# Kernel tuning notes

Hardware: AMD Instinct MI355X
Metric: run time of the kernel (lower is better)

Reference implementation:

```python
import jax, jax.numpy as jnp
import numpy as np

DIM = 512
HEADS = 16
WS = (2, 7, 7)
N = WS[0] * WS[1] * WS[2]  # 98
NW = 64  # number of windows in mask
B_ = 512  # num_windows * batch
HEAD_DIM = DIM // HEADS
SCALE = HEAD_DIM ** -0.5
TABLE = (2 * WS[0] - 1) * (2 * WS[1] - 1) * (2 * WS[2] - 1)  # 507


def _relative_position_index():
    # Faithful to the repo (note: middle coord is NOT multiplied by (2*Ww-1),
    # matching the source exactly).
    ct, ch, cw = np.arange(WS[0]), np.arange(WS[1]), np.arange(WS[2])
    coords = np.stack(np.meshgrid(ct, ch, cw, indexing='ij'))  # [3,Th,Tw,Tw]
    flat = coords.reshape(3, -1)  # [3,N]
    rel = flat[:, :, None] - flat[:, None, :]  # [3,N,N]
    rel = rel.transpose(1, 2, 0).copy()  # [N,N,3]
    rel[:, :, 0] += WS[0] - 1
    rel[:, :, 1] += WS[1] - 1
    rel[:, :, 2] += WS[2] - 1
    rel[:, :, 0] *= (2 * WS[1] - 1) * (2 * WS[2] - 1)
    return rel.sum(-1).astype(np.int32)  # [N,N]


def setup_inputs() -> dict:
    key = jax.random.key(0)
    ks = jax.random.split(key, 7)
    x = jax.random.normal(ks[0], (B_, N, DIM), dtype=jnp.float32)
    mask = jnp.zeros((NW, N, N), dtype=jnp.float32)
    qkv_w = jax.random.normal(ks[1], (3 * DIM, DIM), dtype=jnp.float32) * (DIM ** -0.5)
    qkv_b = jnp.zeros((3 * DIM,), dtype=jnp.float32)
    proj_w = jax.random.normal(ks[2], (DIM, DIM), dtype=jnp.float32) * (DIM ** -0.5)
    proj_b = jnp.zeros((DIM,), dtype=jnp.float32)
    bias_table = jax.random.normal(ks[3], (TABLE, HEADS), dtype=jnp.float32) * 0.02
    rel_index = jnp.asarray(_relative_position_index())
    return {"x": x, "mask": mask, "qkv_w": qkv_w, "qkv_b": qkv_b,
            "proj_w": proj_w, "proj_b": proj_b, "bias_table": bias_table,
            "rel_index": rel_index}


def reference(x, mask, qkv_w, qkv_b, proj_w, proj_b, bias_table, rel_index):
    Bw, n, c = x.shape
    # QKV projection -> [3, B_, H, N, hd]
    qkv = (x @ qkv_w.T + qkv_b).reshape(Bw, n, 3, HEADS, HEAD_DIM)
    qkv = qkv.transpose(2, 0, 3, 1, 4)
    q, k, v = qkv[0], qkv[1], qkv[2]
    attn = jnp.einsum('bhnd,bhmd->bhnm', q * SCALE, k)  # [B_,H,N,N]
    # Gathered relative position bias -> [H,N,N]
    bias = bias_table[rel_index.reshape(-1)].reshape(n, n, HEADS).transpose(2, 0, 1)
    attn = attn + bias[None]
    # Broadcast mask over batch groups of nW windows
    nW = mask.shape[0]
    attn = attn.reshape(Bw // nW, nW, HEADS, n, n) + mask[None, :, None]
    attn = attn.reshape(Bw, HEADS, n, n)
    attn = jax.nn.softmax(attn, axis=-1)
    out = jnp.einsum('bhnm,bhmd->bhnd', attn, v)
    out = out.transpose(0, 2, 1, 3).reshape(Bw, n, c)
    return out @ proj_w.T + proj_b
```

## Files before the change

### kernel.cpp

```cpp
#include <hip/hip_runtime.h>
#include <stdint.h>

#define HEADS 16
#define NTOK 98
#define HD 32
#define SCALE_Q 0.17677669529663687f

typedef __attribute__((ext_vector_type(4))) float floatx4;
typedef __attribute__((ext_vector_type(8))) short shortx8;

__device__ __forceinline__ unsigned short f2bf(float f) {
  union { float f; unsigned u; } v; v.f = f;
  unsigned r = v.u + 0x7fffu + ((v.u >> 16) & 1u);
  return (unsigned short)(r >> 16);
}
__device__ __forceinline__ float bf2f(unsigned short s) {
  union { unsigned u; float f; } v; v.u = ((unsigned)s) << 16;
  return v.f;
}

__device__ __forceinline__ void gload_lds16(const void* g, void* l) {
  __builtin_amdgcn_global_load_lds(
      (const __attribute__((address_space(1))) unsigned int*)g,
      (__attribute__((address_space(3))) unsigned int*)l, 16, 0, 0);
}

__global__ void convert_x_kernel(const float* __restrict__ x,
                                 unsigned short* __restrict__ xbf) {
  int idx = blockIdx.x * 256 + threadIdx.x;
  const float4 f0 = *(const float4*)(x + (size_t)idx * 8);
  const float4 f1 = *(const float4*)(x + (size_t)idx * 8 + 4);
  union { ushort us[8]; uint4 u4; } pk;
  pk.us[0] = f2bf(f0.x); pk.us[1] = f2bf(f0.y);
  pk.us[2] = f2bf(f0.z); pk.us[3] = f2bf(f0.w);
  pk.us[4] = f2bf(f1.x); pk.us[5] = f2bf(f1.y);
  pk.us[6] = f2bf(f1.z); pk.us[7] = f2bf(f1.w);
  *(uint4*)(xbf + (size_t)idx * 8) = pk.u4;
}

__global__ void convert_w_kernel(const float* __restrict__ qkv_w,
                                 const float* __restrict__ proj_w,
                                 unsigned short* __restrict__ wq,
                                 unsigned short* __restrict__ wp) {
  int idx = blockIdx.x * 256 + threadIdx.x;
  if (idx < 1536 * 512) wq[idx] = f2bf(qkv_w[idx]);
  if (idx < 512 * 512) wp[idx] = f2bf(proj_w[idx]);
}

__global__ void bmprep_kernel(const float* __restrict__ table,
                              const int* __restrict__ rel,
                              const float* __restrict__ mask,
                              unsigned short* __restrict__ biasF,
                              unsigned short* __restrict__ maskF) {
  int idx = blockIdx.x * 256 + threadIdx.x;
  if (idx < 229376) {
    int e = idx & 31, lane = (idx >> 5) & 63;
    int rest = idx >> 11;
    int mt = rest % 7, h = rest / 7;
    int nt = e >> 2, r = e & 3;
    int i = mt * 16 + ((lane >> 4) << 2) + r;
    int j = (nt << 4) + (lane & 15);
    int ii = i < NTOK ? i : 97, jj = j < NTOK ? j : 97;
    float v = (nt < 7) ? table[rel[ii * NTOK + jj] * HEADS + h] : 0.f;
    biasF[idx] = f2bf(v);
  } else {
    int t = idx - 229376;
    int e = t & 31, lane = (t >> 5) & 63;
    int rest = t >> 11;
    int mt = rest % 7, wdx = rest / 7;
    int nt = e >> 2, r = e & 3;
    int i = mt * 16 + ((lane >> 4) << 2) + r;
    int j = (nt << 4) + (lane & 15);
    float v;
    if (nt >= 7) v = 0.f;
    else if (j >= NTOK) v = -1e30f;
    else {
      int ii = i < NTOK ? i : 97;
      v = mask[wdx * (NTOK * NTOK) + ii * NTOK + j];
    }
    maskF[t] = f2bf(v);
  }
}

__global__ __launch_bounds__(512, 2)
void qkv_gemm_kernel(const unsigned short* __restrict__ xbf,
                     const unsigned short* __restrict__ wbf,
                     const float* __restrict__ qkv_b,
                     unsigned short* __restrict__ q_out,
                     unsigned short* __restrict__ k_out,
                     unsigned short* __restrict__ v_out) {
  __shared__ unsigned short As[3][128 * 32];
  __shared__ unsigned short Bs[3][256 * 32];
  const int tid = threadIdx.x;
  const int wave = tid >> 6, lane = tid & 63;
  const int id = blockIdx.x;
  const int xc = id & 7, tt = id >> 3;
  const int m0 = (xc * 49 + tt / 6) * 128, n0 = (tt % 6) * 256;
  const int wm = wave & 1, wn = wave >> 1;
  const int ln15 = lane & 15, qd = lane >> 4;
  const int bl_r = lane >> 2, bl_s = lane & 3;

  const int sg_st = bl_s ^ ((bl_r >> 1) & 3);
  const int swz_rd = (qd ^ ((ln15 >> 1) & 3)) * 8;

  const unsigned short* aG = xbf + (size_t)(m0 + wave * 16 + bl_r) * 512 + sg_st * 8;
  const unsigned short* bG0 = wbf + (size_t)(n0 + wave * 32 + bl_r) * 512 + sg_st * 8;
  const unsigned short* bG1 = wbf + (size_t)(n0 + wave * 32 + 16 + bl_r) * 512 + sg_st * 8;

#define QSTAGE(bufi, kk)                                                        \
  do {                                                                          \
    gload_lds16((const void*)(aG + (kk)), (void*)&As[bufi][wave * 512]);        \
    gload_lds16((const void*)(bG0 + (kk)), (void*)&Bs[bufi][wave * 1024]);      \
    gload_lds16((const void*)(bG1 + (kk)), (void*)&Bs[bufi][wave * 1024 + 512]);\
  } while (0)

  QSTAGE(0, 0);
  QSTAGE(1, 32);

  floatx4 acc[4][4] = {};
#pragma unroll
  for (int it = 0; it < 16; ++it) {
    if (it == 15) asm volatile("s_waitcnt vmcnt(0)" ::: "memory");
    else          asm volatile("s_waitcnt vmcnt(3)" ::: "memory");
    __builtin_amdgcn_sched_barrier(0);
    __builtin_amdgcn_s_barrier();
    __builtin_amdgcn_sched_barrier(0);
    if (it + 2 < 16) QSTAGE((it + 2) % 3, (it + 2) * 32);
    const unsigned short* Ab = As[it % 3];
    const unsigned short* Bb = Bs[it % 3];
    shortx8 afrag[4], bfrag[4];
#pragma unroll
    for (int mt = 0; mt < 4; ++mt)
      afrag[mt] = *(const shortx8*)&Ab[(wm * 64 + mt * 16 + ln15) * 32 + swz_rd];
#pragma unroll
    for (int nt = 0; nt < 4; ++nt)
      bfrag[nt] = *(const shortx8*)&Bb[(wn * 64 + nt * 16 + ln15) * 32 + swz_rd];
    __builtin_amdgcn_s_setprio(1);
#pragma unroll
    for (int mt = 0; mt < 4; ++mt)
#pragma unroll
      for (int nt = 0; nt < 4; ++nt)
        acc[mt][nt] = __builtin_amdgcn_mfma_f32_16x16x32_bf16(
            afrag[mt], bfrag[nt], acc[mt][nt], 0, 0, 0);
    __builtin_amdgcn_s_setprio(0);
  }
#undef QSTAGE

  const int which = n0 >> 9;
  unsigned short* __restrict__ outp =
      (which == 0) ? q_out : ((which == 1) ? k_out : v_out);
  const float sc = (which == 0) ? SCALE_Q : 1.0f;
#pragma unroll
  for (int mt = 0; mt < 4; ++mt) {
#pragma unroll
    for (int r = 0; r < 4; ++r) {
      int grow = m0 + wm * 64 + mt * 16 + qd * 4 + r;
      unsigned b = (unsigned)grow / 98u;
      unsigned i = (unsigned)grow - b * 98u;
#pragma unroll
      for (int nt = 0; nt < 4; ++nt) {
        int col = n0 + wn * 64 + nt * 16 + ln15;
        float val = (acc[mt][nt][r] + qkv_b[col]) * sc;
        int h = (col >> 5) & 15;
        int d = col & 31;
        size_t oidx = ((size_t)(b * 16 + h) * 98 + i) * 32 + d;
        outp[oidx] = f2bf(val);
      }
    }
  }
}

__global__ __launch_bounds__(448, 6)
void attn_kernel(const unsigned short* __restrict__ qg,
                 const unsigned short* __restrict__ kg,
                 const unsigned short* __restrict__ vg,
                 const unsigned short* __restrict__ biasF,
                 const unsigned short* __restrict__ maskF,
                 unsigned short* __restrict__ outg) {
  __shared__ __align__(16) unsigned short Vt[32 * 136];
  __shared__ __align__(16) unsigned short Ps[7][1928];
  const int tid = threadIdx.x;
  const int bh = blockIdx.x;
  const int b = bh >> 4, h = bh & 15, w = b & 63;
  const size_t base = (size_t)bh * (NTOK * HD);
  const int wave = tid >> 6, lane = tid & 63;
  const int ln15 = lane & 15, qd = lane >> 4;

  for (int idx = tid; idx < 544; idx += 448)
    ((uint4*)Vt)[idx] = make_uint4(0, 0, 0, 0);
  for (int idx = tid; idx < 1687; idx += 448)
    ((uint4*)Ps)[idx] = make_uint4(0, 0, 0, 0);
  __syncthreads();
  for (int t = tid; t < 392; t += 448) {
    int i = t >> 2, seg = t & 3;
    union { uint4 u4; unsigned short us[8]; } u;
    u.u4 = *(const uint4*)(vg + base + i * 32 + seg * 8);
    int d0 = seg * 8;
#pragma unroll
    for (int e0 = 0; e0 < 8; ++e0) {
      int e = (e0 + seg * 2) & 7;
      Vt[(d0 + e) * 136 + i] = u.us[e];
    }
  }
  __syncthreads();

  const int mt = wave;
  const shortx8* bB = (const shortx8*)(biasF + (((size_t)h * 7 + mt) * 64 + lane) * 32);
  const shortx8* mB = (const shortx8*)(maskF + (((size_t)w * 7 + mt) * 64 + lane) * 32);
  shortx8 bias_c[4], mask_c[4];
#pragma unroll
  for (int c = 0; c < 4; ++c) { bias_c[c] = bB[c]; mask_c[c] = mB[c]; }

  shortx8 af = *(const shortx8*)(qg + base + (mt * 16 + ln15) * 32 + qd * 8);
  floatx4 sacc[7];
  __builtin_amdgcn_s_setprio(1);
#pragma unroll
  for (int nt = 0; nt < 7; ++nt) {
    shortx8 bf = *(const shortx8*)(kg + base + (nt * 16 + ln15) * 32 + qd * 8);
    floatx4 z = {};
    sacc[nt] = __builtin_amdgcn_mfma_f32_16x16x32_bf16(af, bf, z, 0, 0, 0);
  }
  __builtin_amdgcn_s_setprio(0);
#pragma unroll
  for (int nt = 0; nt < 7; ++nt)
#pragma unroll
    for (int r = 0; r < 4; ++r) {
      int ee = nt * 4 + r, c = ee >> 3, el = ee & 7;
      sacc[nt][r] += bf2f((unsigned short)bias_c[c][el]) +
                     bf2f((unsigned short)mask_c[c][el]);
    }

  float linv[4];
#pragma unroll
  for (int r = 0; r < 4; ++r) {
    float mx = sacc[0][r];
#pragma unroll
    for (int nt = 1; nt < 7; ++nt) mx = fmaxf(mx, sacc[nt][r]);
#pragma unroll
    for (int off = 1; off < 16; off <<= 1)
      mx = fmaxf(mx, __shfl_xor(mx, off, 64));
    float sum = 0.f;
#pragma unroll
    for (int nt = 0; nt < 7; ++nt) {
      float p = __expf(sacc[nt][r] - mx);
      sacc[nt][r] = p;
      sum += p;
    }
#pragma unroll
    for (int off = 1; off < 16; off <<= 1) sum += __shfl_xor(sum, off, 64);
    linv[r] = 1.0f / sum;
  }

  unsigned short* Pw = Ps[wave];
#pragma unroll
  for (int nt = 0; nt < 7; ++nt)
#pragma unroll
    for (int r = 0; r < 4; ++r)
      Pw[(qd * 4 + r) * 120 + nt * 16 + ln15] = f2bf(sacc[nt][r]);

  floatx4 o0 = {}, o1 = {};
  __builtin_amdgcn_s_setprio(1);
#pragma unroll
  for (int ks = 0; ks < 4; ++ks) {
    shortx8 ap = *(const shortx8*)&Pw[ln15 * 120 + ks * 32 + qd * 8];
    shortx8 bv0 = *(const shortx8*)&Vt[ln15 * 136 + ks * 32 + qd * 8];
    shortx8 bv1 = *(const shortx8*)&Vt[(16 + ln15) * 136 + ks * 32 + qd * 8];
    o0 = __builtin_amdgcn_mfma_f32_16x16x32_bf16(ap, bv0, o0, 0, 0, 0);
    o1 = __builtin_amdgcn_mfma_f32_16x16x32_bf16(ap, bv1, o1, 0, 0, 0);
  }
  __builtin_amdgcn_s_setprio(0);
#pragma unroll
  for (int r = 0; r < 4; ++r) {
    int i = mt * 16 + qd * 4 + r;
    if (i < NTOK) {
      size_t ob = ((size_t)b * NTOK + i) * 512 + h * 32;
      outg[ob + ln15] = f2bf(o0[r] * linv[r]);
      outg[ob + 16 + ln15] = f2bf(o1[r] * linv[r]);
    }
  }
}

__global__ __launch_bounds__(256, 3)
void proj_gemm_kernel(const unsigned short* __restrict__ a,
                      const unsigned short* __restrict__ wbf,
                      const float* __restrict__ proj_b,
                      float* __restrict__ out) {
  __shared__ unsigned short As[3][128 * 32];
  __shared__ unsigned short Bs[3][128 * 32];
  const int tid = threadIdx.x;
  const int wave = tid >> 6, lane = tid & 63;
  const int id = blockIdx.x;
  const int xc = id & 7, tt = id >> 3;
  const int m0 = (xc * 49 + (tt >> 2)) * 128, n0 = (tt & 3) * 128;
  const int wm = wave & 1, wn = wave >> 1;
  const int ln15 = lane & 15, qd = lane >> 4;
  const int bl_r = lane >> 2, bl_s = lane & 3;

  const int sg_st = bl_s ^ ((bl_r >> 1) & 3);
  const int swz_rd = (qd ^ ((ln15 >> 1) & 3)) * 8;

  const unsigned short* aG0 = a + (size_t)(m0 + wave * 32 + bl_r) * 512 + sg_st * 8;
  const unsigned short* aG1 = aG0 + (size_t)16 * 512;
  const unsigned short* bG0 = wbf + (size_t)(n0 + wave * 32 + bl_r) * 512 + sg_st * 8;
  const unsigned short* bG1 = bG0 + (size_t)16 * 512;

#define PSTAGE(bufi, kk)                                                         \
  do {                                                                           \
    gload_lds16((const void*)(aG0 + (kk)), (void*)&As[bufi][wave * 1024]);       \
    gload_lds16((const void*)(aG1 + (kk)), (void*)&As[bufi][wave * 1024 + 512]); \
    gload_lds16((const void*)(bG0 + (kk)), (void*)&Bs[bufi][wave * 1024]);       \
    gload_lds16((const void*)(bG1 + (kk)), (void*)&Bs[bufi][wave * 1024 + 512]); \
  } while (0)

  PSTAGE(0, 0);
  PSTAGE(1, 32);

  floatx4 acc[4][4] = {};
#pragma unroll
  for (int it = 0; it < 16; ++it) {
    if (it == 15) asm volatile("s_waitcnt vmcnt(0)" ::: "memory");
    else          asm volatile("s_waitcnt vmcnt(4)" ::: "memory");
    __builtin_amdgcn_sched_barrier(0);
    __builtin_amdgcn_s_barrier();
    __builtin_amdgcn_sched_barrier(0);
    if (it + 2 < 16) PSTAGE((it + 2) % 3, (it + 2) * 32);
    const unsigned short* Ab = As[it % 3];
    const unsigned short* Bb = Bs[it % 3];
    shortx8 afrag[4], bfrag[4];
#pragma unroll
    for (int mt = 0; mt < 4; ++mt)
      afrag[mt] = *(const shortx8*)&Ab[(wm * 64 + mt * 16 + ln15) * 32 + swz_rd];
#pragma unroll
    for (int nt = 0; nt < 4; ++nt)
      bfrag[nt] = *(const shortx8*)&Bb[(wn * 64 + nt * 16 + ln15) * 32 + swz_rd];
    __builtin_amdgcn_s_setprio(1);
#pragma unroll
    for (int mt = 0; mt < 4; ++mt)
#pragma unroll
      for (int nt = 0; nt < 4; ++nt)
        acc[mt][nt] = __builtin_amdgcn_mfma_f32_16x16x32_bf16(
            afrag[mt], bfrag[nt], acc[mt][nt], 0, 0, 0);
    __builtin_amdgcn_s_setprio(0);
  }
#undef PSTAGE

#pragma unroll
  for (int mt = 0; mt < 4; ++mt) {
#pragma unroll
    for (int r = 0; r < 4; ++r) {
      int grow = m0 + wm * 64 + mt * 16 + qd * 4 + r;
#pragma unroll
      for (int nt = 0; nt < 4; ++nt) {
        int col = n0 + wn * 64 + nt * 16 + ln15;
        out[(size_t)grow * 512 + col] = acc[mt][nt][r] + proj_b[col];
      }
    }
  }
}

extern "C" void kernel_launch(void* const* d_in, const int* in_sizes, int n_in,
                              void* d_out, int out_size, void* d_ws, size_t ws_size,
                              hipStream_t stream) {
  const float* x          = (const float*)d_in[0];
  const float* mask       = (const float*)d_in[1];
  const float* qkv_w      = (const float*)d_in[2];
  const float* qkv_b      = (const float*)d_in[3];
  const float* proj_w     = (const float*)d_in[4];
  const float* proj_b     = (const float*)d_in[5];
  const float* bias_table = (const float*)d_in[6];
  const int*   rel_index  = (const int*)d_in[7];
  float* out = (float*)d_out;

  char* ws = (char*)d_ws;
  unsigned short* ws_qkvw  = (unsigned short*)(ws + 0);
  unsigned short* ws_projw = (unsigned short*)(ws + 1572864);
  unsigned short* ws_biasF = (unsigned short*)(ws + 2097152);
  unsigned short* ws_maskF = (unsigned short*)(ws + 2555904);
  unsigned short* ws_q     = (unsigned short*)(ws + 4390912);
  unsigned short* ws_k     = (unsigned short*)(ws + 55771136);
  unsigned short* ws_v     = (unsigned short*)(ws + 107151360);
  unsigned short* ws_attn  = (unsigned short*)(ws + 158531584);
  unsigned short* ws_xbf   = ws_attn;

  hipLaunchKernelGGL(convert_x_kernel, dim3(12544), dim3(256), 0, stream,
                     x, ws_xbf);
  hipLaunchKernelGGL(convert_w_kernel, dim3(3072), dim3(256), 0, stream,
                     qkv_w, proj_w, ws_qkvw, ws_projw);
  hipLaunchKernelGGL(bmprep_kernel, dim3(4480), dim3(256), 0, stream,
                     bias_table, rel_index, mask, ws_biasF, ws_maskF);
  hipLaunchKernelGGL(qkv_gemm_kernel, dim3(2352), dim3(512), 0, stream,
                     ws_xbf, ws_qkvw, qkv_b, ws_q, ws_k, ws_v);
  hipLaunchKernelGGL(attn_kernel, dim3(8192), dim3(448), 0, stream,
                     ws_q, ws_k, ws_v, ws_biasF, ws_maskF, ws_attn);
  hipLaunchKernelGGL(proj_gemm_kernel, dim3(1568), dim3(256), 0, stream,
                     ws_attn, ws_projw, proj_b, out);
}
```

Measured before the change: 426.7 us.

## Fuse prep kernels and use 4-wave QKV GEMM with 64x128 wave tiles

Merges the x conversion, weight conversion and bias/mask preparation into a single prep kernel launch to cut launch overhead. Reorganizes the QKV GEMM from 8 waves with 64x64 wave tiles to 4 waves with 64x128 wave tiles, so each wave issues more global-to-LDS loads per stage and reuses A fragments across more MFMAs. Register pressure doubles for accumulators and there are fewer waves per block to hide latency.

```diff
diff --git a/kernel.cpp b/kernel.cpp
--- a/kernel.cpp
+++ b/kernel.cpp
@@ -25,64 +25,65 @@
       (__attribute__((address_space(3))) unsigned int*)l, 16, 0, 0);
 }
 
-__global__ void convert_x_kernel(const float* __restrict__ x,
-                                 unsigned short* __restrict__ xbf) {
-  int idx = blockIdx.x * 256 + threadIdx.x;
-  const float4 f0 = *(const float4*)(x + (size_t)idx * 8);
-  const float4 f1 = *(const float4*)(x + (size_t)idx * 8 + 4);
-  union { ushort us[8]; uint4 u4; } pk;
-  pk.us[0] = f2bf(f0.x); pk.us[1] = f2bf(f0.y);
-  pk.us[2] = f2bf(f0.z); pk.us[3] = f2bf(f0.w);
-  pk.us[4] = f2bf(f1.x); pk.us[5] = f2bf(f1.y);
-  pk.us[6] = f2bf(f1.z); pk.us[7] = f2bf(f1.w);
-  *(uint4*)(xbf + (size_t)idx * 8) = pk.u4;
-}
-
-__global__ void convert_w_kernel(const float* __restrict__ qkv_w,
-                                 const float* __restrict__ proj_w,
-                                 unsigned short* __restrict__ wq,
-                                 unsigned short* __restrict__ wp) {
-  int idx = blockIdx.x * 256 + threadIdx.x;
-  if (idx < 1536 * 512) wq[idx] = f2bf(qkv_w[idx]);
-  if (idx < 512 * 512) wp[idx] = f2bf(proj_w[idx]);
-}
-
-__global__ void bmprep_kernel(const float* __restrict__ table,
-                              const int* __restrict__ rel,
-                              const float* __restrict__ mask,
-                              unsigned short* __restrict__ biasF,
-                              unsigned short* __restrict__ maskF) {
-  int idx = blockIdx.x * 256 + threadIdx.x;
-  if (idx < 229376) {
-    int e = idx & 31, lane = (idx >> 5) & 63;
-    int rest = idx >> 11;
-    int mt = rest % 7, h = rest / 7;
-    int nt = e >> 2, r = e & 3;
-    int i = mt * 16 + ((lane >> 4) << 2) + r;
-    int j = (nt << 4) + (lane & 15);
-    int ii = i < NTOK ? i : 97, jj = j < NTOK ? j : 97;
-    float v = (nt < 7) ? table[rel[ii * NTOK + jj] * HEADS + h] : 0.f;
-    biasF[idx] = f2bf(v);
+__global__ void prep_kernel(const float* __restrict__ x,
+                            const float* __restrict__ qkv_w,
+                            const float* __restrict__ proj_w,
+                            const float* __restrict__ table,
+                            const int* __restrict__ rel,
+                            const float* __restrict__ mask,
+                            unsigned short* __restrict__ xbf,
+                            unsigned short* __restrict__ wq,
+                            unsigned short* __restrict__ wp,
+                            unsigned short* __restrict__ biasF,
+                            unsigned short* __restrict__ maskF) {
+  const int bid = blockIdx.x, tid = threadIdx.x;
+  if (bid < 12544) {
+    int idx = bid * 256 + tid;
+    const float4 f0 = *(const float4*)(x + (size_t)idx * 8);
+    const float4 f1 = *(const float4*)(x + (size_t)idx * 8 + 4);
+    union { ushort us[8]; uint4 u4; } pk;
+    pk.us[0] = f2bf(f0.x); pk.us[1] = f2bf(f0.y);
+    pk.us[2] = f2bf(f0.z); pk.us[3] = f2bf(f0.w);
+    pk.us[4] = f2bf(f1.x); pk.us[5] = f2bf(f1.y);
+    pk.us[6] = f2bf(f1.z); pk.us[7] = f2bf(f1.w);
+    *(uint4*)(xbf + (size_t)idx * 8) = pk.u4;
+  } else if (bid < 15616) {
+    int idx = (bid - 12544) * 256 + tid;
+    if (idx < 1536 * 512) wq[idx] = f2bf(qkv_w[idx]);
+    if (idx < 512 * 512) wp[idx] = f2bf(proj_w[idx]);
   } else {
-    int t = idx - 229376;
-    int e = t & 31, lane = (t >> 5) & 63;
-    int rest = t >> 11;
-    int mt = rest % 7, wdx = rest / 7;
-    int nt = e >> 2, r = e & 3;
-    int i = mt * 16 + ((lane >> 4) << 2) + r;
-    int j = (nt << 4) + (lane & 15);
-    float v;
-    if (nt >= 7) v = 0.f;
-    else if (j >= NTOK) v = -1e30f;
-    else {
-      int ii = i < NTOK ? i : 97;
-      v = mask[wdx * (NTOK * NTOK) + ii * NTOK + j];
-    }
-    maskF[t] = f2bf(v);
-  }
-}
-
-__global__ __launch_bounds__(512, 2)
+    int idx = (bid - 15616) * 256 + tid;
+    if (idx < 229376) {
+      int e = idx & 31, lane = (idx >> 5) & 63;
+      int rest = idx >> 11;
+      int mt = rest % 7, h = rest / 7;
+      int nt = e >> 2, r = e & 3;
+      int i = mt * 16 + ((lane >> 4) << 2) + r;
+      int j = (nt << 4) + (lane & 15);
+      int ii = i < NTOK ? i : 97, jj = j < NTOK ? j : 97;
+      float v = (nt < 7) ? table[rel[ii * NTOK + jj] * HEADS + h] : 0.f;
+      biasF[idx] = f2bf(v);
+    } else {
+      int t = idx - 229376;
+      int e = t & 31, lane = (t >> 5) & 63;
+      int rest = t >> 11;
+      int mt = rest % 7, wdx = rest / 7;
+      int nt = e >> 2, r = e & 3;
+      int i = mt * 16 + ((lane >> 4) << 2) + r;
+      int j = (nt << 4) + (lane & 15);
+      float v;
+      if (nt >= 7) v = 0.f;
+      else if (j >= NTOK) v = -1e30f;
+      else {
+        int ii = i < NTOK ? i : 97;
+        v = mask[wdx * (NTOK * NTOK) + ii * NTOK + j];
+      }
+      maskF[t] = f2bf(v);
+    }
+  }
+}
+
+__global__ __launch_bounds__(256, 2)
 void qkv_gemm_kernel(const unsigned short* __restrict__ xbf,
                      const unsigned short* __restrict__ wbf,
                      const float* __restrict__ qkv_b,
@@ -103,43 +104,49 @@
   const int sg_st = bl_s ^ ((bl_r >> 1) & 3);
   const int swz_rd = (qd ^ ((ln15 >> 1) & 3)) * 8;
 
-  const unsigned short* aG = xbf + (size_t)(m0 + wave * 16 + bl_r) * 512 + sg_st * 8;
-  const unsigned short* bG0 = wbf + (size_t)(n0 + wave * 32 + bl_r) * 512 + sg_st * 8;
-  const unsigned short* bG1 = wbf + (size_t)(n0 + wave * 32 + 16 + bl_r) * 512 + sg_st * 8;
-
-#define QSTAGE(bufi, kk)                                                        \
-  do {                                                                          \
-    gload_lds16((const void*)(aG + (kk)), (void*)&As[bufi][wave * 512]);        \
-    gload_lds16((const void*)(bG0 + (kk)), (void*)&Bs[bufi][wave * 1024]);      \
-    gload_lds16((const void*)(bG1 + (kk)), (void*)&Bs[bufi][wave * 1024 + 512]);\
+  const unsigned short* aG0 = xbf + (size_t)(m0 + wave * 16 + bl_r) * 512 + sg_st * 8;
+  const unsigned short* aG1 = aG0 + (size_t)64 * 512;
+  const unsigned short* bG0 = wbf + (size_t)(n0 + wave * 16 + bl_r) * 512 + sg_st * 8;
+
+#define QSTAGE(bufi, kk)                                                          \
+  do {                                                                            \
+    gload_lds16((const void*)(aG0 + (kk)), (void*)&As[bufi][wave * 512]);         \
+    gload_lds16((const void*)(aG1 + (kk)), (void*)&As[bufi][2048 + wave * 512]);  \
+    gload_lds16((const void*)(bG0 + (kk)), (void*)&Bs[bufi][wave * 512]);         \
+    gload_lds16((const void*)(bG0 + (size_t)64 * 512 + (kk)),                     \
+                (void*)&Bs[bufi][2048 + wave * 512]);                             \
+    gload_lds16((const void*)(bG0 + (size_t)128 * 512 + (kk)),                    \
+                (void*)&Bs[bufi][4096 + wave * 512]);                             \
+    gload_lds16((const void*)(bG0 + (size_t)192 * 512 + (kk)),                    \
+                (void*)&Bs[bufi][6144 + wave * 512]);                             \
   } while (0)
 
   QSTAGE(0, 0);
   QSTAGE(1, 32);
 
-  floatx4 acc[4][4] = {};
+  floatx4 acc[4][8] = {};
 #pragma unroll
   for (int it = 0; it < 16; ++it) {
     if (it == 15) asm volatile("s_waitcnt vmcnt(0)" ::: "memory");
-    else          asm volatile("s_waitcnt vmcnt(3)" ::: "memory");
+    else          asm volatile("s_waitcnt vmcnt(6)" ::: "memory");
     __builtin_amdgcn_sched_barrier(0);
     __builtin_amdgcn_s_barrier();
     __builtin_amdgcn_sched_barrier(0);
     if (it + 2 < 16) QSTAGE((it + 2) % 3, (it + 2) * 32);
     const unsigned short* Ab = As[it % 3];
     const unsigned short* Bb = Bs[it % 3];
-    shortx8 afrag[4], bfrag[4];
+    shortx8 afrag[4], bfrag[8];
 #pragma unroll
     for (int mt = 0; mt < 4; ++mt)
       afrag[mt] = *(const shortx8*)&Ab[(wm * 64 + mt * 16 + ln15) * 32 + swz_rd];
 #pragma unroll
-    for (int nt = 0; nt < 4; ++nt)
-      bfrag[nt] = *(const shortx8*)&Bb[(wn * 64 + nt * 16 + ln15) * 32 + swz_rd];
+    for (int nt = 0; nt < 8; ++nt)
+      bfrag[nt] = *(const shortx8*)&Bb[(wn * 128 + nt * 16 + ln15) * 32 + swz_rd];
     __builtin_amdgcn_s_setprio(1);
 #pragma unroll
     for (int mt = 0; mt < 4; ++mt)
 #pragma unroll
-      for (int nt = 0; nt < 4; ++nt)
+      for (int nt = 0; nt < 8; ++nt)
         acc[mt][nt] = __builtin_amdgcn_mfma_f32_16x16x32_bf16(
             afrag[mt], bfrag[nt], acc[mt][nt], 0, 0, 0);
     __builtin_amdgcn_s_setprio(0);
@@ -158,8 +165,8 @@
       unsigned b = (unsigned)grow / 98u;
       unsigned i = (unsigned)grow - b * 98u;
 #pragma unroll
-      for (int nt = 0; nt < 4; ++nt) {
-        int col = n0 + wn * 64 + nt * 16 + ln15;
+      for (int nt = 0; nt < 8; ++nt) {
+        int col = n0 + wn * 128 + nt * 16 + ln15;
         float val = (acc[mt][nt][r] + qkv_b[col]) * sc;
         int h = (col >> 5) & 15;
         int d = col & 31;
@@ -382,13 +389,10 @@
   unsigned short* ws_attn  = (unsigned short*)(ws + 158531584);
   unsigned short* ws_xbf   = ws_attn;
 
-  hipLaunchKernelGGL(convert_x_kernel, dim3(12544), dim3(256), 0, stream,
-                     x, ws_xbf);
-  hipLaunchKernelGGL(convert_w_kernel, dim3(3072), dim3(256), 0, stream,
-                     qkv_w, proj_w, ws_qkvw, ws_projw);
-  hipLaunchKernelGGL(bmprep_kernel, dim3(4480), dim3(256), 0, stream,
-                     bias_table, rel_index, mask, ws_biasF, ws_maskF);
-  hipLaunchKernelGGL(qkv_gemm_kernel, dim3(2352), dim3(512), 0, stream,
+  hipLaunchKernelGGL(prep_kernel, dim3(20096), dim3(256), 0, stream,
+                     x, qkv_w, proj_w, bias_table, rel_index, mask,
+                     ws_xbf, ws_qkvw, ws_projw, ws_biasF, ws_maskF);
+  hipLaunchKernelGGL(qkv_gemm_kernel, dim3(2352), dim3(256), 0, stream,
                      ws_xbf, ws_qkvw, qkv_b, ws_q, ws_k, ws_v);
   hipLaunchKernelGGL(attn_kernel, dim3(8192), dim3(448), 0, stream,
                      ws_q, ws_k, ws_v, ws_biasF, ws_maskF, ws_attn);
```

Result: slower. 449.0 us (+5.2%).
